# Kernel optimization log

Measured on AMD Instinct MI355X. Metric: run time of the kernel, lower is better.

## Reference

```python
import jax, jax.numpy as jnp
import numpy as np

B, JX, JM, D, H = 8, 2048, 2048, 512, 512
NEG_INF = -1e30


def setup_inputs() -> dict:
    key = jax.random.key(0)
    ks = jax.random.split(key, 6)
    inputs = jax.random.normal(ks[0], (B, JX, D), dtype=jnp.float32)
    memory = jax.random.normal(ks[1], (B, JM, D), dtype=jnp.float32)
    mask = jax.random.randint(ks[2], (B, JM), 0, 2, dtype=jnp.int32)
    # guarantee at least one valid memory slot per row
    mask = mask.at[:, 0].set(1)
    Wq = jax.random.normal(ks[3], (D, H), dtype=jnp.float32) * 0.05
    Wk = jax.random.normal(ks[4], (D, H), dtype=jnp.float32) * 0.05
    Wg = jax.random.normal(ks[5], (2 * D, 2 * D), dtype=jnp.float32) * 0.05
    return {"inputs": inputs, "memory": memory, "mask": mask,
            "Wq": Wq, "Wk": Wk, "Wg": Wg}


def reference(inputs, memory, mask, Wq, Wk, Wg):
    hidden = Wq.shape[-1]
    # two ReLU projections (no bias)
    q = jax.nn.relu(jnp.einsum('bxd,dh->bxh', inputs, Wq))   # [B,JX,H]
    k = jax.nn.relu(jnp.einsum('bmd,dh->bmh', memory, Wk))   # [B,JM,H]
    # scaled dot-product scores
    scores = jnp.einsum('bxh,bmh->bxm', q, k) / (hidden ** 0.5)  # [B,JX,JM]
    # softmax_mask: -inf where mask == 0 (broadcast over JX instead of tile)
    m = mask[:, None, :].astype(scores.dtype)                 # [B,1,JM]
    scores = scores * m + (1.0 - m) * NEG_INF
    logits = jax.nn.softmax(scores, axis=-1)                  # [B,JX,JM]
    # attend over RAW memory (not projected)
    att = jnp.einsum('bxm,bmd->bxd', logits, memory)          # [B,JX,D]
    # gate combiner: concat -> dense(sigmoid, no bias) -> multiply
    res = jnp.concatenate([inputs, att], axis=-1)             # [B,JX,2D]
    g = jax.nn.sigmoid(jnp.einsum('bxe,ef->bxf', res, Wg))
    return res * g
```

## Files before the change

### kernel.cpp

```cpp
#include <hip/hip_runtime.h>

typedef unsigned short u16;
typedef unsigned int   u32;

typedef short s16x8 __attribute__((ext_vector_type(8)));
typedef float f32x4 __attribute__((ext_vector_type(4)));

static __device__ __forceinline__ u16 f2bf(float f) {
  u32 u = __float_as_uint(f);
  u = (u + 0x7fffu + ((u >> 16) & 1u)) >> 16;
  return (u16)u;
}
static __device__ __forceinline__ float bf2f(u16 h) {
  return __uint_as_float(((u32)h) << 16);
}
static __device__ __forceinline__ f32x4 mfma16(s16x8 a, s16x8 b, f32x4 c) {
  return __builtin_amdgcn_mfma_f32_16x16x32_bf16(a, b, c, 0, 0, 0);
}
static __device__ __forceinline__ void gload16(const u16* g, u16* l) {
  __builtin_amdgcn_global_load_lds(
      (const __attribute__((address_space(1))) void*)g,
      (__attribute__((address_space(3))) void*)l, 16, 0, 0);
}

#define WAITVM0() asm volatile("s_waitcnt vmcnt(0)" ::: "memory")
#define BAR()                                  \
  do {                                         \
    asm volatile("" ::: "memory");             \
    __builtin_amdgcn_s_barrier();              \
    asm volatile("" ::: "memory");             \
  } while (0)

__global__ __launch_bounds__(256) void cvt_k(const float* __restrict__ in,
                                             u16* __restrict__ out, int n8) {
  int i = blockIdx.x * 256 + threadIdx.x;
  if (i >= n8) return;
  const float4* p = reinterpret_cast<const float4*>(in);
  float4 a = p[2 * i], b = p[2 * i + 1];
  union { u16 u[8]; uint4 v; } r;
  r.u[0] = f2bf(a.x); r.u[1] = f2bf(a.y); r.u[2] = f2bf(a.z); r.u[3] = f2bf(a.w);
  r.u[4] = f2bf(b.x); r.u[5] = f2bf(b.y); r.u[6] = f2bf(b.z); r.u[7] = f2bf(b.w);
  reinterpret_cast<uint4*>(out)[i] = r.v;
}

__global__ void tcvt_k(const float* __restrict__ in, u16* __restrict__ out,
                       int R, int C, long long ibs, long long obs) {
  __shared__ float t[32][33];
  const float* ip = in + (size_t)blockIdx.z * ibs;
  u16* op = out + (size_t)blockIdx.z * obs;
  int r0 = blockIdx.y * 32, c0 = blockIdx.x * 32;
  int x = threadIdx.x, y = threadIdx.y;
  for (int i = y; i < 32; i += 8) t[i][x] = ip[(size_t)(r0 + i) * C + c0 + x];
  __syncthreads();
  for (int i = y; i < 32; i += 8) op[(size_t)(c0 + i) * R + r0 + x] = f2bf(t[x][i]);
}

__global__ __launch_bounds__(256) void softmax_k(u16* __restrict__ P,
                                                 const int* __restrict__ mask,
                                                 float scale) {
  __shared__ float redm[4], reds[4];
  const int row = blockIdx.x;
  const int bb = row >> 11;
  const int tid = threadIdx.x;
  u16* p = P + (size_t)row * 4096;
  const int* mk = mask + (size_t)bb * 2048;
  uint4 raw = reinterpret_cast<const uint4*>(p)[tid];
  int4 ma = reinterpret_cast<const int4*>(mk)[2 * tid];
  int4 mc = reinterpret_cast<const int4*>(mk)[2 * tid + 1];
  float v[8];
  v[0] = ma.x ? bf2f((u16)(raw.x & 0xffff)) * scale : -1e30f;
  v[1] = ma.y ? bf2f((u16)(raw.x >> 16))    * scale : -1e30f;
  v[2] = ma.z ? bf2f((u16)(raw.y & 0xffff)) * scale : -1e30f;
  v[3] = ma.w ? bf2f((u16)(raw.y >> 16))    * scale : -1e30f;
  v[4] = mc.x ? bf2f((u16)(raw.z & 0xffff)) * scale : -1e30f;
  v[5] = mc.y ? bf2f((u16)(raw.z >> 16))    * scale : -1e30f;
  v[6] = mc.z ? bf2f((u16)(raw.w & 0xffff)) * scale : -1e30f;
  v[7] = mc.w ? bf2f((u16)(raw.w >> 16))    * scale : -1e30f;
  float mx = v[0];
  #pragma unroll
  for (int i = 1; i < 8; ++i) mx = fmaxf(mx, v[i]);
  for (int off = 32; off; off >>= 1) mx = fmaxf(mx, __shfl_xor(mx, off));
  if ((tid & 63) == 0) redm[tid >> 6] = mx;
  __syncthreads();
  mx = fmaxf(fmaxf(redm[0], redm[1]), fmaxf(redm[2], redm[3]));
  float sum = 0.f;
  #pragma unroll
  for (int i = 0; i < 8; ++i) { v[i] = __expf(v[i] - mx); sum += v[i]; }
  for (int off = 32; off; off >>= 1) sum += __shfl_xor(sum, off);
  if ((tid & 63) == 0) reds[tid >> 6] = sum;
  __syncthreads();
  sum = reds[0] + reds[1] + reds[2] + reds[3];
  float inv = 1.0f / sum;
  union { u16 u[8]; uint4 q; } r;
  #pragma unroll
  for (int i = 0; i < 8; ++i) r.u[i] = f2bf(v[i] * inv);
  reinterpret_cast<uint4*>(p)[tid] = r.q;
}

template <int EPI>
__global__ __launch_bounds__(512, 2) void gemm8p_k(
    const u16* __restrict__ A, const u16* __restrict__ A2,
    const u16* __restrict__ Bt, const u16* __restrict__ Bt2,
    float* __restrict__ Cf, u16* __restrict__ Cb,
    const float* __restrict__ R0, const u16* __restrict__ R1,
    int N, int K, int lda, int ldb, int ldc, int Ksplit, int Msp,
    int nx, int ny, int nwg,
    long long A_bs, long long B_bs, long long C_bs) {
  __shared__ u16 As[2][256 * 64];
  __shared__ u16 Bs[2][256 * 64];
  const int bid = blockIdx.x;
  const int wgid = (bid & 7) * (nwg >> 3) + (bid >> 3);
  const int bx = wgid % nx;
  const int by = (wgid / nx) % ny;
  const int bz = wgid / (nx * ny);
  const int tid = threadIdx.x;
  const int wave = tid >> 6, lane = tid & 63;
  const size_t Aoff = (size_t)bz * A_bs;
  const size_t Boff = (size_t)bz * B_bs;
  const size_t Coff = (size_t)bz * C_bs;
  const int m0 = by * 256, n0 = bx * 256;
  const int wr = wave >> 2, wc = wave & 3;
  const int l15 = lane & 15, l4 = lane >> 4;
  const int srow = lane >> 3;
  const int scolsw = (((lane & 7) ^ (lane >> 3)) << 3);
  const int rsw = (l15 & 7) << 3;
  const u16* Bbase = ((m0 < Msp) ? Bt : Bt2) + Boff;

  f32x4 acc[8][4];
  #pragma unroll
  for (int i = 0; i < 8; ++i)
    #pragma unroll
    for (int j = 0; j < 4; ++j) acc[i][j] = (f32x4){0.f, 0.f, 0.f, 0.f};

  const int nt = K / 64;
  auto stageTile = [&](int buf, int k0) {
    const u16* Abase; int kloc;
    if (k0 < Ksplit) { Abase = A + Aoff;  kloc = k0; }
    else             { Abase = A2 + Aoff; kloc = k0 - Ksplit; }
    #pragma unroll
    for (int c = 0; c < 4; ++c) {
      int chunk = wave * 4 + c;
      int row = chunk * 8 + srow;
      gload16(Abase + (size_t)(m0 + row) * lda + kloc + scolsw, &As[buf][chunk * 512]);
      gload16(Bbase + (size_t)(n0 + row) * ldb + k0 + scolsw,   &Bs[buf][chunk * 512]);
    }
  };

  stageTile(0, 0);
  WAITVM0();
  BAR();

  for (int t = 0; t < nt; ++t) {
    const int b = t & 1;
    if (t + 1 < nt) stageTile(b ^ 1, (t + 1) * 64);
    s16x8 bfr[4][2];
    #pragma unroll
    for (int ni = 0; ni < 4; ++ni)
      #pragma unroll
      for (int kk = 0; kk < 2; ++kk)
        bfr[ni][kk] = *reinterpret_cast<const s16x8*>(
            &Bs[b][(wc * 64 + ni * 16 + l15) * 64 + ((kk * 32 + l4 * 8) ^ rsw)]);
    #pragma unroll
    for (int q = 0; q < 4; ++q) {
      s16x8 af[2][2];
      #pragma unroll
      for (int mi2 = 0; mi2 < 2; ++mi2)
        #pragma unroll
        for (int kk = 0; kk < 2; ++kk)
          af[mi2][kk] = *reinterpret_cast<const s16x8*>(
              &As[b][(wr * 128 + (q * 2 + mi2) * 16 + l15) * 64 +
                     ((kk * 32 + l4 * 8) ^ rsw)]);
      BAR();
      __builtin_amdgcn_s_setprio(1);
      #pragma unroll
      for (int mi2 = 0; mi2 < 2; ++mi2)
        #pragma unroll
        for (int ni = 0; ni < 4; ++ni)
          #pragma unroll
          for (int kk = 0; kk < 2; ++kk)
            acc[q * 2 + mi2][ni] = mfma16(af[mi2][kk], bfr[ni][kk], acc[q * 2 + mi2][ni]);
      __builtin_amdgcn_s_setprio(0);
      if (q < 3) BAR();
    }
    WAITVM0();
    BAR();
  }

  #pragma unroll
  for (int mi = 0; mi < 8; ++mi) {
    #pragma unroll
    for (int ni = 0; ni < 4; ++ni) {
      int col = n0 + wc * 64 + ni * 16 + l15;
      #pragma unroll
      for (int j = 0; j < 4; ++j) {
        int row = m0 + wr * 128 + mi * 16 + l4 * 4 + j;
        float v = acc[mi][ni][j];
        size_t cidx = Coff + (size_t)row * ldc + col;
        if (EPI == 0) {
          Cb[cidx] = f2bf(fmaxf(v, 0.f));
        } else if (EPI == 1) {
          Cb[cidx] = f2bf(v);
        } else {
          float r = (col < Ksplit) ? R0[(size_t)row * 512 + col]
                                   : bf2f(R1[(size_t)row * 512 + (col - 512)]);
          float g = 1.0f / (1.0f + __expf(-v));
          Cf[cidx] = r * g;
        }
      }
    }
  }
}

__global__ __launch_bounds__(256, 2) void gemm_pm_k(const u16* __restrict__ P,
                                                    const u16* __restrict__ MT,
                                                    u16* __restrict__ C) {
  __shared__ u16 As[2][128 * 64];
  __shared__ u16 Bs[2][128 * 64];
  const int l = blockIdx.x;
  const int logical = (l & 7) * 64 + (l >> 3);
  const int n0 = (logical & 3) * 128;
  const int m0 = ((logical >> 2) & 15) * 128;
  const int z = logical >> 6;
  const u16* Ab = P + (size_t)z * 2048 * 4096;
  const u16* Bb = MT + (size_t)z * 512 * 2048;
  u16* Cb = C + (size_t)z * 2048 * 512;
  const int tid = threadIdx.x, wave = tid >> 6, lane = tid & 63;
  const int wr = wave >> 1, wc = wave & 1;
  const int l15 = lane & 15, l4 = lane >> 4;
  const int srow = lane >> 3;
  const int scolsw = (((lane & 7) ^ (lane >> 3)) << 3);
  const int rsw = (l15 & 7) << 3;

  f32x4 acc[4][4];
  #pragma unroll
  for (int i = 0; i < 4; ++i)
    #pragma unroll
    for (int j = 0; j < 4; ++j) acc[i][j] = (f32x4){0.f, 0.f, 0.f, 0.f};

  auto stage = [&](int buf, int k0) {
    #pragma unroll
    for (int c = 0; c < 4; ++c) {
      int chunk = wave * 4 + c;
      int row = chunk * 8 + srow;
      gload16(Ab + (size_t)(m0 + row) * 4096 + k0 + scolsw, &As[buf][chunk * 512]);
      gload16(Bb + (size_t)(n0 + row) * 2048 + k0 + scolsw, &Bs[buf][chunk * 512]);
    }
  };
  auto compute = [&](int cur) {
    __builtin_amdgcn_s_setprio(1);
    #pragma unroll
    for (int kk = 0; kk < 64; kk += 32) {
      s16x8 af[4], bfr[4];
      #pragma unroll
      for (int mi = 0; mi < 4; ++mi)
        af[mi] = *reinterpret_cast<const s16x8*>(
            &As[cur][(wr * 64 + mi * 16 + l15) * 64 + (((kk + l4 * 8) ^ rsw))]);
      #pragma unroll
      for (int ni = 0; ni < 4; ++ni)
        bfr[ni] = *reinterpret_cast<const s16x8*>(
            &Bs[cur][(wc * 64 + ni * 16 + l15) * 64 + (((kk + l4 * 8) ^ rsw))]);
      #pragma unroll
      for (int mi = 0; mi < 4; ++mi)
        #pragma unroll
        for (int ni = 0; ni < 4; ++ni)
          acc[mi][ni] = mfma16(af[mi], bfr[ni], acc[mi][ni]);
    }
    __builtin_amdgcn_s_setprio(0);
  };

  const int nt = 32;
  stage(0, 0);
  stage(1, 64);
  asm volatile("s_waitcnt vmcnt(8)" ::: "memory");
  BAR();
  for (int t = 0; t < nt; ++t) {
    const int cur = t & 1;
    compute(cur);
    BAR();
    if (t + 2 < nt) stage(cur, (t + 2) * 64);
    if (t + 1 < nt) {
      if (t + 2 < nt) { asm volatile("s_waitcnt vmcnt(8)" ::: "memory"); }
      else            { WAITVM0(); }
      BAR();
    }
  }

  #pragma unroll
  for (int mi = 0; mi < 4; ++mi) {
    #pragma unroll
    for (int ni = 0; ni < 4; ++ni) {
      int col = n0 + wc * 64 + ni * 16 + l15;
      #pragma unroll
      for (int j = 0; j < 4; ++j) {
        int row = m0 + wr * 64 + mi * 16 + l4 * 4 + j;
        Cb[(size_t)row * 512 + col] = f2bf(acc[mi][ni][j]);
      }
    }
  }
}

extern "C" void kernel_launch(void* const* d_in, const int* in_sizes, int n_in,
                              void* d_out, int out_size, void* d_ws, size_t ws_size,
                              hipStream_t stream) {
  const float* inputs = (const float*)d_in[0];
  const float* memory = (const float*)d_in[1];
  const int*   mask   = (const int*)d_in[2];
  const float* Wq     = (const float*)d_in[3];
  const float* Wk     = (const float*)d_in[4];
  const float* Wg     = (const float*)d_in[5];
  float* out = (float*)d_out;

  char* ws = (char*)d_ws;
  size_t off = 0;
  auto alloc = [&](size_t bytes) {
    void* p = ws + off;
    off += (bytes + 255) & ~(size_t)255;
    return p;
  };
  u16* in_b  = (u16*)alloc(16384ULL * 512 * 2);
  u16* mem_b = (u16*)alloc(16384ULL * 512 * 2);
  u16* memT  = (u16*)alloc(16384ULL * 512 * 2);
  u16* WqT   = (u16*)alloc(512ULL * 512 * 2);
  u16* WkT   = (u16*)alloc(512ULL * 512 * 2);
  u16* WgT   = (u16*)alloc(1024ULL * 1024 * 2);
  u16* q_b   = (u16*)alloc(16384ULL * 512 * 2);
  u16* k_b   = (u16*)alloc(16384ULL * 512 * 2);
  u16* sc    = (u16*)alloc(8ULL * 2048 * 4096 * 2);
  u16* att_b = (u16*)alloc(16384ULL * 512 * 2);
  (void)ws_size; (void)in_sizes; (void)n_in; (void)out_size;

  const int n8 = (16384 * 512) / 8;
  cvt_k<<<(n8 + 255) / 256, 256, 0, stream>>>(inputs, in_b, n8);
  cvt_k<<<(n8 + 255) / 256, 256, 0, stream>>>(memory, mem_b, n8);
  dim3 tb(32, 8);
  tcvt_k<<<dim3(16, 16, 1), tb, 0, stream>>>(Wq, WqT, 512, 512, 0, 0);
  tcvt_k<<<dim3(16, 16, 1), tb, 0, stream>>>(Wk, WkT, 512, 512, 0, 0);
  tcvt_k<<<dim3(32, 32, 1), tb, 0, stream>>>(Wg, WgT, 1024, 1024, 0, 0);
  tcvt_k<<<dim3(16, 64, 8), tb, 0, stream>>>(memory, memT, 2048, 512,
                                             2048LL * 512, 2048LL * 512);

  gemm8p_k<0><<<256, 512, 0, stream>>>(
      in_b, nullptr, WqT, WkT, nullptr, q_b, nullptr, nullptr,
      512, 512, 512, 512, 512, 1 << 30, 16384, 2, 128, 256, 0, 0, 0);

  gemm8p_k<1><<<512, 512, 0, stream>>>(
      q_b, nullptr, k_b, k_b, nullptr, sc, nullptr, nullptr,
      2048, 512, 512, 512, 4096, 1 << 30, 1 << 30, 8, 8, 512,
      2048LL * 512, 2048LL * 512, 2048LL * 4096);

  softmax_k<<<16384, 256, 0, stream>>>(sc, mask, 0.044194173824159216f);

  gemm_pm_k<<<512, 256, 0, stream>>>(sc, memT, att_b);

  gemm8p_k<3><<<256, 512, 0, stream>>>(
      in_b, att_b, WgT, WgT, out, nullptr, inputs, att_b,
      1024, 1024, 512, 1024, 1024, 512, 1 << 30, 4, 64, 256, 0, 0, 0);
}
```

Baseline: 280.8 us.

## Replace 256-tile GEMMs with templated 128-tile kernels and shrink score buffer stride

Swaps the double-buffered 256x256 GEMM for a templated 128x128, 256-thread GEMM with compile-time sizes and a single LDS buffer synchronized by __syncthreads. The score buffer row stride drops from 4096 to 2048, which halves the workspace and makes softmax and the PM GEMM rows contiguous. The memory bf16 copy now lands right after the inputs copy so the projection GEMM reads one contiguous A. This gives more workgroups but loses load/compute overlap and reuse from the larger tile.

```diff
diff --git a/kernel.cpp b/kernel.cpp
--- a/kernel.cpp
+++ b/kernel.cpp
@@ -22,14 +22,6 @@
       (const __attribute__((address_space(1))) void*)g,
       (__attribute__((address_space(3))) void*)l, 16, 0, 0);
 }
-
-#define WAITVM0() asm volatile("s_waitcnt vmcnt(0)" ::: "memory")
-#define BAR()                                  \
-  do {                                         \
-    asm volatile("" ::: "memory");             \
-    __builtin_amdgcn_s_barrier();              \
-    asm volatile("" ::: "memory");             \
-  } while (0)
 
 __global__ __launch_bounds__(256) void cvt_k(const float* __restrict__ in,
                                              u16* __restrict__ out, int n8) {
@@ -62,7 +54,7 @@
   const int row = blockIdx.x;
   const int bb = row >> 11;
   const int tid = threadIdx.x;
-  u16* p = P + (size_t)row * 4096;
+  u16* p = P + (size_t)row * 2048;
   const int* mk = mask + (size_t)bb * 2048;
   uint4 raw = reinterpret_cast<const uint4*>(p)[tid];
   int4 ma = reinterpret_cast<const int4*>(mk)[2 * tid];
@@ -97,112 +89,88 @@
   reinterpret_cast<uint4*>(p)[tid] = r.q;
 }
 
-template <int EPI>
-__global__ __launch_bounds__(512, 2) void gemm8p_k(
+template <int EPI, int NT, int NX, int NY,
+          int LDA, int LDB, int LDC, int KSPLIT, int MSPLIT,
+          long long ABS, long long BBS, long long CBS, int NWG>
+__global__ __launch_bounds__(256) void g128(
     const u16* __restrict__ A, const u16* __restrict__ A2,
     const u16* __restrict__ Bt, const u16* __restrict__ Bt2,
     float* __restrict__ Cf, u16* __restrict__ Cb,
-    const float* __restrict__ R0, const u16* __restrict__ R1,
-    int N, int K, int lda, int ldb, int ldc, int Ksplit, int Msp,
-    int nx, int ny, int nwg,
-    long long A_bs, long long B_bs, long long C_bs) {
-  __shared__ u16 As[2][256 * 64];
-  __shared__ u16 Bs[2][256 * 64];
+    const float* __restrict__ R0, const u16* __restrict__ R1) {
+  __shared__ u16 As[128 * 64];
+  __shared__ u16 Bs[128 * 64];
   const int bid = blockIdx.x;
-  const int wgid = (bid & 7) * (nwg >> 3) + (bid >> 3);
-  const int bx = wgid % nx;
-  const int by = (wgid / nx) % ny;
-  const int bz = wgid / (nx * ny);
+  const int wgid = (bid & 7) * (NWG / 8) + (bid >> 3);
+  const int bx = wgid % NX;
+  const int by = (wgid / NX) % NY;
+  const int bz = wgid / (NX * NY);
   const int tid = threadIdx.x;
   const int wave = tid >> 6, lane = tid & 63;
-  const size_t Aoff = (size_t)bz * A_bs;
-  const size_t Boff = (size_t)bz * B_bs;
-  const size_t Coff = (size_t)bz * C_bs;
-  const int m0 = by * 256, n0 = bx * 256;
-  const int wr = wave >> 2, wc = wave & 3;
+  const int m0 = by * 128, n0 = bx * 128;
+  const int wr = wave >> 1, wc = wave & 1;
   const int l15 = lane & 15, l4 = lane >> 4;
   const int srow = lane >> 3;
   const int scolsw = (((lane & 7) ^ (lane >> 3)) << 3);
   const int rsw = (l15 & 7) << 3;
-  const u16* Bbase = ((m0 < Msp) ? Bt : Bt2) + Boff;
-
-  f32x4 acc[8][4];
-  #pragma unroll
-  for (int i = 0; i < 8; ++i)
+  const u16* Bbase = ((m0 < MSPLIT) ? Bt : Bt2) + (size_t)bz * BBS;
+
+  f32x4 acc[4][4];
+  #pragma unroll
+  for (int i = 0; i < 4; ++i)
     #pragma unroll
     for (int j = 0; j < 4; ++j) acc[i][j] = (f32x4){0.f, 0.f, 0.f, 0.f};
 
-  const int nt = K / 64;
-  auto stageTile = [&](int buf, int k0) {
-    const u16* Abase; int kloc;
-    if (k0 < Ksplit) { Abase = A + Aoff;  kloc = k0; }
-    else             { Abase = A2 + Aoff; kloc = k0 - Ksplit; }
+  for (int t = 0; t < NT; ++t) {
+    const int k0 = t * 64;
+    const u16* Ab;
+    int kl;
+    if (k0 < KSPLIT) { Ab = A + (size_t)bz * ABS;  kl = k0; }
+    else             { Ab = A2 + (size_t)bz * ABS; kl = k0 - KSPLIT; }
+    __syncthreads();
     #pragma unroll
     for (int c = 0; c < 4; ++c) {
       int chunk = wave * 4 + c;
       int row = chunk * 8 + srow;
-      gload16(Abase + (size_t)(m0 + row) * lda + kloc + scolsw, &As[buf][chunk * 512]);
-      gload16(Bbase + (size_t)(n0 + row) * ldb + k0 + scolsw,   &Bs[buf][chunk * 512]);
-    }
-  };
-
-  stageTile(0, 0);
-  WAITVM0();
-  BAR();
-
-  for (int t = 0; t < nt; ++t) {
-    const int b = t & 1;
-    if (t + 1 < nt) stageTile(b ^ 1, (t + 1) * 64);
-    s16x8 bfr[4][2];
-    #pragma unroll
-    for (int ni = 0; ni < 4; ++ni)
-      #pragma unroll
-      for (int kk = 0; kk < 2; ++kk)
-        bfr[ni][kk] = *reinterpret_cast<const s16x8*>(
-            &Bs[b][(wc * 64 + ni * 16 + l15) * 64 + ((kk * 32 + l4 * 8) ^ rsw)]);
-    #pragma unroll
-    for (int q = 0; q < 4; ++q) {
-      s16x8 af[2][2];
-      #pragma unroll
-      for (int mi2 = 0; mi2 < 2; ++mi2)
-        #pragma unroll
-        for (int kk = 0; kk < 2; ++kk)
-          af[mi2][kk] = *reinterpret_cast<const s16x8*>(
-              &As[b][(wr * 128 + (q * 2 + mi2) * 16 + l15) * 64 +
-                     ((kk * 32 + l4 * 8) ^ rsw)]);
-      BAR();
-      __builtin_amdgcn_s_setprio(1);
-      #pragma unroll
-      for (int mi2 = 0; mi2 < 2; ++mi2)
+      gload16(Ab + (size_t)(m0 + row) * LDA + kl + scolsw, &As[chunk * 512]);
+      gload16(Bbase + (size_t)(n0 + row) * LDB + k0 + scolsw, &Bs[chunk * 512]);
+    }
+    __syncthreads();
+    #pragma unroll
+    for (int kk = 0; kk < 64; kk += 32) {
+      s16x8 af[4], bfr[4];
+      #pragma unroll
+      for (int mi = 0; mi < 4; ++mi)
+        af[mi] = *reinterpret_cast<const s16x8*>(
+            &As[(wr * 64 + mi * 16 + l15) * 64 + ((kk + l4 * 8) ^ rsw)]);
+      #pragma unroll
+      for (int ni = 0; ni < 4; ++ni)
+        bfr[ni] = *reinterpret_cast<const s16x8*>(
+            &Bs[(wc * 64 + ni * 16 + l15) * 64 + ((kk + l4 * 8) ^ rsw)]);
+      #pragma unroll
+      for (int mi = 0; mi < 4; ++mi)
         #pragma unroll
         for (int ni = 0; ni < 4; ++ni)
-          #pragma unroll
-          for (int kk = 0; kk < 2; ++kk)
-            acc[q * 2 + mi2][ni] = mfma16(af[mi2][kk], bfr[ni][kk], acc[q * 2 + mi2][ni]);
-      __builtin_amdgcn_s_setprio(0);
-      if (q < 3) BAR();
-    }
-    WAITVM0();
-    BAR();
+          acc[mi][ni] = mfma16(af[mi], bfr[ni], acc[mi][ni]);
+    }
   }
 
   #pragma unroll
-  for (int mi = 0; mi < 8; ++mi) {
+  for (int mi = 0; mi < 4; ++mi) {
     #pragma unroll
     for (int ni = 0; ni < 4; ++ni) {
       int col = n0 + wc * 64 + ni * 16 + l15;
       #pragma unroll
       for (int j = 0; j < 4; ++j) {
-        int row = m0 + wr * 128 + mi * 16 + l4 * 4 + j;
+        int row = m0 + wr * 64 + mi * 16 + l4 * 4 + j;
         float v = acc[mi][ni][j];
-        size_t cidx = Coff + (size_t)row * ldc + col;
+        size_t cidx = (size_t)bz * CBS + (size_t)row * LDC + col;
         if (EPI == 0) {
           Cb[cidx] = f2bf(fmaxf(v, 0.f));
         } else if (EPI == 1) {
           Cb[cidx] = f2bf(v);
         } else {
-          float r = (col < Ksplit) ? R0[(size_t)row * 512 + col]
-                                   : bf2f(R1[(size_t)row * 512 + (col - 512)]);
+          float r = (col < 512) ? R0[(size_t)row * 512 + col]
+                                : bf2f(R1[(size_t)row * 512 + (col - 512)]);
           float g = 1.0f / (1.0f + __expf(-v));
           Cf[cidx] = r * g;
         }
@@ -221,7 +189,7 @@
   const int n0 = (logical & 3) * 128;
   const int m0 = ((logical >> 2) & 15) * 128;
   const int z = logical >> 6;
-  const u16* Ab = P + (size_t)z * 2048 * 4096;
+  const u16* Ab = P + (size_t)z * 2048 * 2048;
   const u16* Bb = MT + (size_t)z * 512 * 2048;
   u16* Cb = C + (size_t)z * 2048 * 512;
   const int tid = threadIdx.x, wave = tid >> 6, lane = tid & 63;
@@ -242,7 +210,7 @@
     for (int c = 0; c < 4; ++c) {
       int chunk = wave * 4 + c;
       int row = chunk * 8 + srow;
-      gload16(Ab + (size_t)(m0 + row) * 4096 + k0 + scolsw, &As[buf][chunk * 512]);
+      gload16(Ab + (size_t)(m0 + row) * 2048 + k0 + scolsw, &As[buf][chunk * 512]);
       gload16(Bb + (size_t)(n0 + row) * 2048 + k0 + scolsw, &Bs[buf][chunk * 512]);
     }
   };
@@ -272,16 +240,16 @@
   stage(0, 0);
   stage(1, 64);
   asm volatile("s_waitcnt vmcnt(8)" ::: "memory");
-  BAR();
+  __builtin_amdgcn_s_barrier();
   for (int t = 0; t < nt; ++t) {
     const int cur = t & 1;
     compute(cur);
-    BAR();
+    __builtin_amdgcn_s_barrier();
     if (t + 2 < nt) stage(cur, (t + 2) * 64);
     if (t + 1 < nt) {
       if (t + 2 < nt) { asm volatile("s_waitcnt vmcnt(8)" ::: "memory"); }
-      else            { WAITVM0(); }
-      BAR();
+      else            { asm volatile("s_waitcnt vmcnt(0)" ::: "memory"); }
+      __builtin_amdgcn_s_barrier();
     }
   }
 
@@ -325,13 +293,13 @@
   u16* WgT   = (u16*)alloc(1024ULL * 1024 * 2);
   u16* q_b   = (u16*)alloc(16384ULL * 512 * 2);
   u16* k_b   = (u16*)alloc(16384ULL * 512 * 2);
-  u16* sc    = (u16*)alloc(8ULL * 2048 * 4096 * 2);
+  u16* sc    = (u16*)alloc(8ULL * 2048 * 2048 * 2);
   u16* att_b = (u16*)alloc(16384ULL * 512 * 2);
-  (void)ws_size; (void)in_sizes; (void)n_in; (void)out_size;
+  (void)ws_size; (void)in_sizes; (void)n_in; (void)out_size; (void)mem_b;
 
   const int n8 = (16384 * 512) / 8;
   cvt_k<<<(n8 + 255) / 256, 256, 0, stream>>>(inputs, in_b, n8);
-  cvt_k<<<(n8 + 255) / 256, 256, 0, stream>>>(memory, mem_b, n8);
+  cvt_k<<<(n8 + 255) / 256, 256, 0, stream>>>(memory, in_b + 16384ULL * 512, n8);
   dim3 tb(32, 8);
   tcvt_k<<<dim3(16, 16, 1), tb, 0, stream>>>(Wq, WqT, 512, 512, 0, 0);
   tcvt_k<<<dim3(16, 16, 1), tb, 0, stream>>>(Wk, WkT, 512, 512, 0, 0);
@@ -339,20 +307,20 @@
   tcvt_k<<<dim3(16, 64, 8), tb, 0, stream>>>(memory, memT, 2048, 512,
                                              2048LL * 512, 2048LL * 512);
 
-  gemm8p_k<0><<<256, 512, 0, stream>>>(
-      in_b, nullptr, WqT, WkT, nullptr, q_b, nullptr, nullptr,
-      512, 512, 512, 512, 512, 1 << 30, 16384, 2, 128, 256, 0, 0, 0);
-
-  gemm8p_k<1><<<512, 512, 0, stream>>>(
-      q_b, nullptr, k_b, k_b, nullptr, sc, nullptr, nullptr,
-      2048, 512, 512, 512, 4096, 1 << 30, 1 << 30, 8, 8, 512,
-      2048LL * 512, 2048LL * 512, 2048LL * 4096);
+  g128<0, 8, 4, 256, 512, 512, 512, (1 << 30), 16384, 0, 0, 0, 1024>
+      <<<1024, 256, 0, stream>>>(in_b, nullptr, WqT, WkT,
+                                 nullptr, q_b, nullptr, nullptr);
+
+  g128<1, 8, 16, 16, 512, 512, 2048, (1 << 30), (1 << 30),
+       2048LL * 512, 2048LL * 512, 2048LL * 2048, 2048>
+      <<<2048, 256, 0, stream>>>(q_b, nullptr, k_b, k_b,
+                                 nullptr, sc, nullptr, nullptr);
 
   softmax_k<<<16384, 256, 0, stream>>>(sc, mask, 0.044194173824159216f);
 
   gemm_pm_k<<<512, 256, 0, stream>>>(sc, memT, att_b);
 
-  gemm8p_k<3><<<256, 512, 0, stream>>>(
-      in_b, att_b, WgT, WgT, out, nullptr, inputs, att_b,
-      1024, 1024, 512, 1024, 1024, 512, 1 << 30, 4, 64, 256, 0, 0, 0);
-}
+  g128<3, 16, 8, 128, 512, 1024, 1024, 512, (1 << 30), 0, 0, 0, 1024>
+      <<<1024, 256, 0, stream>>>(in_b, att_b, WgT, WgT,
+                                 out, nullptr, inputs, att_b);
+}
```

Measured after the change: 268.4 us. -4.4%, faster.
